# Optimization experiments

Measured on AMD Instinct MI355X. Metric: run time of the kernel, lower is better.

Reference implementation:

```python
import jax, jax.numpy as jnp
import numpy as np

B, N, H, DH = 2, 512, 12, 64
DIM, DPAIR, DCOND = 768, 128, 512
INNER = 4 * DIM  # expansion_factor * dim


def _ln(x, eps=1e-5):
    m = jnp.mean(x, -1, keepdims=True)
    v = jnp.mean((x - m) ** 2, -1, keepdims=True)
    return (x - m) * jax.lax.rsqrt(v + eps)


def _rope(t):
    # t: [b,h,n,d]; standard rotary over head dim
    d = t.shape[-1]
    pos = jnp.arange(t.shape[2], dtype=t.dtype)
    inv = 1.0 / (10000.0 ** (jnp.arange(0, d, 2, dtype=t.dtype) / d))
    ang = pos[:, None] * inv[None, :]  # [n, d/2]
    cos, sin = jnp.cos(ang), jnp.sin(ang)
    t1, t2 = t[..., 0::2], t[..., 1::2]
    return jnp.stack([t1 * cos - t2 * sin, t1 * sin + t2 * cos], -1).reshape(t.shape)


def _adaln(x, cond, mask, gw, gb, bw):
    cn = _ln(cond)
    return (_ln(x) * jax.nn.sigmoid(cn @ gw + gb) + cn @ bw) * mask[..., None]


def _scale_out(x, cond, mask, w, b):
    # adaLN-zero style output scaling
    return x * jax.nn.sigmoid(_ln(cond) @ w + b) * mask[..., None]


def _windowed_attn(q, k, v, bias, pair_mask, n_queries, n_keys):
    # q/k/v: [b,h,n,d]; bias: [b,h,n,n]; pair_mask: [b,n,n]
    b, h, n, d = q.shape
    nw = n // n_queries
    centers = jnp.arange(nw) * n_queries + n_queries // 2
    idx = centers[:, None] - n_keys // 2 + jnp.arange(n_keys)[None, :]  # [nw,nk]
    valid = (idx >= 0) & (idx < n)
    idxc = jnp.clip(idx, 0, n - 1)
    qw = q.reshape(b, h, nw, n_queries, d)
    kw = k[:, :, idxc]  # [b,h,nw,nk,d]
    vw = v[:, :, idxc]
    ib = jnp.broadcast_to(idxc[None, None, :, None, :], (b, h, nw, n_queries, n_keys))
    bias_w = jnp.take_along_axis(bias.reshape(b, h, nw, n_queries, n), ib, axis=-1)
    pm = jnp.take_along_axis(
        pair_mask.reshape(b, nw, n_queries, n),
        jnp.broadcast_to(idxc[None, :, None, :], (b, nw, n_queries, n_keys)), axis=-1)
    scores = jnp.einsum('bhwqd,bhwkd->bhwqk', qw, kw) / jnp.sqrt(jnp.asarray(d, q.dtype)) + bias_w
    ok = (pm[:, None] > 0) & valid[None, None, :, None, :]
    attn = jax.nn.softmax(jnp.where(ok, scores, -1e9), axis=-1)
    out = jnp.einsum('bhwqk,bhwkd->bhwqd', attn, vw)
    return out.reshape(b, h, n, d)


def setup_inputs() -> dict:
    key = jax.random.key(0)
    ks = iter(jax.random.split(key, 48))
    nrm = lambda shape: jax.random.normal(next(ks), shape, jnp.float32) * 0.02
    return dict(
        x=jax.random.normal(next(ks), (B, N, DIM), jnp.float32),
        pair_rep=jax.random.normal(next(ks), (B, N, N, DPAIR), jnp.float32),
        cond=jax.random.normal(next(ks), (B, N, DCOND), jnp.float32),
        mask=jnp.ones((B, N), jnp.float32),
        pair_mask=jnp.ones((B, N, N), jnp.float32),
        adaln1_gw=nrm((DCOND, DIM)), adaln1_gb=jnp.zeros((DIM,), jnp.float32), adaln1_bw=nrm((DCOND, DIM)),
        wq=nrm((DIM, H * DH)), bq=jnp.zeros((H * DH,), jnp.float32),
        wk=nrm((DIM, H * DH)), bk=jnp.zeros((H * DH,), jnp.float32),
        wv=nrm((DIM, H * DH)), bv=jnp.zeros((H * DH,), jnp.float32),
        wg=nrm((DIM, H * DH)), bg=jnp.zeros((H * DH,), jnp.float32),
        wb_pair=nrm((DPAIR, H)),
        wo=nrm((H * DH, DIM)), bo=jnp.zeros((DIM,), jnp.float32),
        scale1_w=nrm((DCOND, DIM)), scale1_b=jnp.full((DIM,), -2.0, jnp.float32),
        adaln2_gw=nrm((DCOND, DIM)), adaln2_gb=jnp.zeros((DIM,), jnp.float32), adaln2_bw=nrm((DCOND, DIM)),
        tr_win=nrm((DIM, 2 * INNER)), tr_wout=nrm((INNER, DIM)),
        scale2_w=nrm((DCOND, DIM)), scale2_b=jnp.full((DIM,), -2.0, jnp.float32),
        n_queries=32, n_keys=128,
    )


def reference(x, pair_rep, cond, mask, pair_mask,
              adaln1_gw, adaln1_gb, adaln1_bw,
              wq, bq, wk, bk, wv, bv, wg, bg, wb_pair, wo, bo,
              scale1_w, scale1_b,
              adaln2_gw, adaln2_gb, adaln2_bw,
              tr_win, tr_wout,
              scale2_w, scale2_b,
              n_queries, n_keys):
    b, n, _ = x.shape
    x = x * mask[..., None]

    # --- MHA (adaLN -> pair-biased rotary windowed attention -> adaLN-zero scale) ---
    xa = _adaln(x, cond, mask, adaln1_gw, adaln1_gb, adaln1_bw)
    q = (xa @ wq + bq).reshape(b, n, H, DH).transpose(0, 2, 1, 3)
    k = (xa @ wk + bk).reshape(b, n, H, DH).transpose(0, 2, 1, 3)
    v = (xa @ wv + bv).reshape(b, n, H, DH).transpose(0, 2, 1, 3)
    q, k = _ln(q), _ln(k)      # qk layernorm
    q, k = _rope(q), _rope(k)  # rotary
    bias = jnp.einsum('bijp,ph->bhij', _ln(pair_rep), wb_pair)
    o = _windowed_attn(q, k, v, bias, pair_mask, n_queries, n_keys)
    o = o.transpose(0, 2, 1, 3).reshape(b, n, H * DH)
    attn_out = (o * jax.nn.sigmoid(xa @ wg + bg)) @ wo + bo
    attn_out = _scale_out(attn_out, cond, mask, scale1_w, scale1_b) * mask[..., None]
    x = (attn_out + x) * mask[..., None]  # residual_mha

    # --- Transition (adaLN -> SwiGLU -> adaLN-zero scale) ---
    xt = _adaln(x, cond, mask, adaln2_gw, adaln2_gb, adaln2_bw)
    a, g = jnp.split(xt @ tr_win, 2, axis=-1)
    tr = ((a * jax.nn.silu(g)) @ tr_wout) * mask[..., None]
    tr = _scale_out(tr, cond, mask, scale2_w, scale2_b) * mask[..., None]
    x = (tr + x) * mask[..., None]  # residual_transition
    return x * mask[..., None]
```

## Files before the change

kernel.cpp:

```cpp
#include <hip/hip_runtime.h>
#include <hip/hip_bf16.h>
#include <math.h>
#include <stdint.h>

#define Bc   2
#define Nc   512
#define Hc   12
#define DHc  64
#define DIMc 768
#define DPAIRc 128
#define DCONDc 512
#define INNERc 3072
#define NQc  32
#define NKc  128
#define NWc  (Nc / NQc)

typedef __attribute__((ext_vector_type(8))) short short8;
typedef __attribute__((ext_vector_type(4))) float floatx4;

__device__ inline float wave_sum(float v) {
#pragma unroll
  for (int off = 32; off > 0; off >>= 1) v += __shfl_xor(v, off, 64);
  return v;
}
__device__ inline float wave_max(float v) {
#pragma unroll
  for (int off = 32; off > 0; off >>= 1) v = fmaxf(v, __shfl_xor(v, off, 64));
  return v;
}
__device__ inline float block_sum(float v, float* red) {
  v = wave_sum(v);
  int wv = threadIdx.x >> 6, lane = threadIdx.x & 63;
  __syncthreads();
  if (lane == 0) red[wv] = v;
  __syncthreads();
  return red[0] + red[1] + red[2] + red[3];
}
__device__ inline float sigmoidf(float x) { return 1.0f / (1.0f + expf(-x)); }

__device__ __forceinline__ void gload16(const void* g, void* l) {
  __builtin_amdgcn_global_load_lds(
      reinterpret_cast<__attribute__((address_space(1))) const void*>(
          reinterpret_cast<uintptr_t>(g)),
      reinterpret_cast<__attribute__((address_space(3))) void*>(
          static_cast<uint32_t>(reinterpret_cast<uintptr_t>(l))),
      16, 0, 0);
}

__global__ __launch_bounds__(256) void ln_rows_bf16_k(const float* __restrict__ in,
                                                      __hip_bfloat16* __restrict__ out, int C) {
  __shared__ float red[4];
  int row = blockIdx.x;
  const float* x = in + (size_t)row * C;
  float s = 0.f;
  for (int c = threadIdx.x; c < C; c += 256) s += x[c];
  float mean = block_sum(s, red) / C;
  float vs = 0.f;
  for (int c = threadIdx.x; c < C; c += 256) { float d = x[c] - mean; vs += d * d; }
  float var = block_sum(vs, red) / C;
  float r = rsqrtf(var + 1e-5f);
  for (int c = threadIdx.x; c < C; c += 256)
    out[(size_t)row * C + c] = __float2bfloat16((x[c] - mean) * r);
}

struct TP6 { const float* s0; const float* s1; const float* s2;
             const float* s3; const float* s4; const float* s5; };
__global__ __launch_bounds__(256) void transpose_cast_batch_k(TP6 p,
    __hip_bfloat16* __restrict__ dstBase, int K, int N, int interleave) {
  __shared__ float tile[32][33];
  const float* srcs[6] = {p.s0, p.s1, p.s2, p.s3, p.s4, p.s5};
  const float* src = srcs[blockIdx.z];
  __hip_bfloat16* dst = dstBase + (size_t)blockIdx.z * K * N;
  int k0 = blockIdx.y * 32, n0 = blockIdx.x * 32;
  int t = threadIdx.x;
  int r = t >> 5, c = t & 31;
#pragma unroll
  for (int i = 0; i < 4; ++i) tile[r + i * 8][c] = src[(size_t)(k0 + r + i * 8) * N + n0 + c];
  __syncthreads();
#pragma unroll
  for (int i = 0; i < 4; ++i) {
    int n = n0 + r + i * 8;
    int dr = n;
    if (interleave) {
      int half = N >> 1;
      dr = (n < half) ? (((n >> 4) << 5) + (n & 15))
                      : ((((n - half) >> 4) << 5) + 16 + ((n - half) & 15));
    }
    dst[(size_t)dr * K + k0 + c] = __float2bfloat16(tile[c][r + i * 8]);
  }
}

__global__ __launch_bounds__(256) void concat_bias_k(
    const float* __restrict__ a1_gb, const float* __restrict__ s1_b,
    const float* __restrict__ a2_gb, const float* __restrict__ s2_b,
    const float* __restrict__ bq, const float* __restrict__ bk,
    const float* __restrict__ bv, const float* __restrict__ bg,
    const float* __restrict__ wb_pair,
    float* __restrict__ cb6, float* __restrict__ bqkvg,
    __hip_bfloat16* __restrict__ wbT, float* __restrict__ colsum) {
  int i = blockIdx.x * 256 + threadIdx.x;
  if (i < 6 * DIMc) {
    int seg = i / DIMc, o = i - seg * DIMc;
    float v = 0.f;
    if (seg == 0) v = a1_gb[o];
    else if (seg == 2) v = s1_b[o];
    else if (seg == 3) v = a2_gb[o];
    else if (seg == 5) v = s2_b[o];
    cb6[i] = v;
  }
  if (i < 4 * DIMc) {
    int seg = i / DIMc, o = i - seg * DIMc;
    bqkvg[i] = (seg == 0) ? bq[o] : (seg == 1) ? bk[o] : (seg == 2) ? bv[o] : bg[o];
  }
  if (i < 16 * DPAIRc) {
    int h = i >> 7, c = i & 127;
    wbT[i] = (h < Hc) ? __float2bfloat16(wb_pair[c * Hc + h]) : __float2bfloat16(0.f);
  }
  if (blockIdx.x == 0 && threadIdx.x < 16) {
    int h = threadIdx.x;
    float s = 0.f;
    if (h < Hc)
      for (int c = 0; c < DPAIRc; ++c)
        s += __bfloat162float(__float2bfloat16(wb_pair[c * Hc + h]));
    colsum[h] = s;
  }
}

template <int WNT>
__global__ __launch_bounds__(256) void gemm_bf16_k(
    const __hip_bfloat16* __restrict__ A, const __hip_bfloat16* __restrict__ Bt,
    float* __restrict__ C, int M, int N, int K,
    const float* __restrict__ bias,
    const float* __restrict__ ss, int ssst,
    const float* __restrict__ resid, const float* __restrict__ maskp, int mode) {
  constexpr int TN = 32 * WNT;
  __shared__ __align__(16) __hip_bfloat16 As[2][128 * 32];
  __shared__ __align__(16) __hip_bfloat16 Bs[2][TN * 32];
  int tid = threadIdx.x;
  int lane = tid & 63, wv = tid >> 6;
  int l16 = lane & 15, quad = lane >> 4;
  int m0 = blockIdx.y * 128, n0 = blockIdx.x * TN;
  int wm0 = (wv >> 1) * 64, wn0 = (wv & 1) * (16 * WNT);

  int srow = tid >> 2;
  int skc = (tid & 3) * 8;
  const __hip_bfloat16* Ab  = A  + (size_t)(m0 + srow) * K + skc;
  const __hip_bfloat16* Ab2 = Ab + (size_t)64 * K;
  const __hip_bfloat16* Bb  = Bt + (size_t)(n0 + srow) * K + skc;
  const __hip_bfloat16* Bb2 = Bb + (size_t)64 * K;
  __hip_bfloat16* AsW0 = &As[0][0] + wv * 512;
  __hip_bfloat16* AsW1 = &As[1][0] + wv * 512;
  __hip_bfloat16* BsW0 = &Bs[0][0] + wv * 512;
  __hip_bfloat16* BsW1 = &Bs[1][0] + wv * 512;

  floatx4 acc[4][WNT];
#pragma unroll
  for (int mi = 0; mi < 4; ++mi)
#pragma unroll
    for (int nj = 0; nj < WNT; ++nj) acc[mi][nj] = (floatx4){0.f, 0.f, 0.f, 0.f};

  auto stage = [&](int kk, __hip_bfloat16* AW, __hip_bfloat16* BW) {
    gload16(Ab + kk, AW);
    gload16(Ab2 + kk, AW + 2048);
    if (WNT == 4) {
      gload16(Bb + kk, BW);
      gload16(Bb2 + kk, BW + 2048);
    } else {
      if (wv < 2) gload16(Bb + kk, BW);
    }
  };
  auto compute = [&](const __hip_bfloat16* Asb, const __hip_bfloat16* Bsb) {
    short8 a[4], b[WNT];
#pragma unroll
    for (int mi = 0; mi < 4; ++mi)
      a[mi] = *(const short8*)(const void*)&Asb[(wm0 + mi * 16 + l16) * 32 + quad * 8];
#pragma unroll
    for (int nj = 0; nj < WNT; ++nj)
      b[nj] = *(const short8*)(const void*)&Bsb[(wn0 + nj * 16 + l16) * 32 + quad * 8];
#pragma unroll
    for (int mi = 0; mi < 4; ++mi)
#pragma unroll
      for (int nj = 0; nj < WNT; ++nj)
        acc[mi][nj] = __builtin_amdgcn_mfma_f32_16x16x32_bf16(a[mi], b[nj], acc[mi][nj], 0, 0, 0);
  };

  stage(0, AsW0, BsW0);
  __syncthreads();
  for (int k0 = 0; k0 < K; k0 += 64) {
    if (k0 + 32 < K) stage(k0 + 32, AsW1, BsW1);
    compute(&As[0][0], &Bs[0][0]);
    __syncthreads();
    if (k0 + 64 < K) stage(k0 + 64, AsW0, BsW0);
    compute(&As[1][0], &Bs[1][0]);
    __syncthreads();
  }

  if (mode == 3) {
    if constexpr (WNT >= 2) {
      __hip_bfloat16* Cb = (__hip_bfloat16*)C;
      int halfN = N >> 1;
#pragma unroll
      for (int mi = 0; mi < 4; ++mi) {
#pragma unroll
        for (int njp = 0; njp < WNT / 2; ++njp) {
          int outcol = ((n0 + wn0) >> 1) + njp * 16 + l16;
#pragma unroll
          for (int r = 0; r < 4; ++r) {
            int m = m0 + wm0 + mi * 16 + quad * 4 + r;
            float av = acc[mi][2 * njp][r];
            float gv = acc[mi][2 * njp + 1][r];
            Cb[(size_t)m * halfN + outcol] = __float2bfloat16(av * gv * sigmoidf(gv));
          }
        }
      }
    }
    return;
  }

#pragma unroll
  for (int mi = 0; mi < 4; ++mi) {
#pragma unroll
    for (int nj = 0; nj < WNT; ++nj) {
      int ncol = n0 + wn0 + nj * 16 + l16;
      float bb = bias ? bias[ncol] : 0.f;
#pragma unroll
      for (int r = 0; r < 4; ++r) {
        int m = m0 + wm0 + mi * 16 + quad * 4 + r;
        float v = acc[mi][nj][r] + bb;
        if (mode == 1) {
          float mk = maskp[m];
          v *= sigmoidf(ss[(size_t)m * ssst + ncol]) * mk * mk;
          v = (v + resid[(size_t)m * N + ncol]) * mk;
        } else if (mode == 2) {
          float mk = maskp[m];
          v = v * mk * sigmoidf(ss[(size_t)m * ssst + ncol]) * mk * mk;
          v = (v + resid[(size_t)m * N + ncol]) * mk * mk;
        }
        C[(size_t)m * N + ncol] = v;
      }
    }
  }
}

__global__ __launch_bounds__(256) void adaln_apply_k(
    const float* __restrict__ xin, const float* __restrict__ maskp,
    const float* __restrict__ graw, const float* __restrict__ braw, int ssst,
    __hip_bfloat16* __restrict__ xa, float* __restrict__ xm) {
  __shared__ float red[4];
  int row = blockIdx.x;
  float mk = maskp[row];
  const float* xr = xin + (size_t)row * DIMc;
  float vals[3];
  float s = 0.f;
#pragma unroll
  for (int it = 0; it < 3; ++it) {
    int c = threadIdx.x + it * 256;
    float v = xr[c] * mk;
    vals[it] = v;
    s += v;
  }
  float mean = block_sum(s, red) * (1.0f / DIMc);
  float vs = 0.f;
#pragma unroll
  for (int it = 0; it < 3; ++it) { float d = vals[it] - mean; vs += d * d; }
  float var = block_sum(vs, red) * (1.0f / DIMc);
  float r = rsqrtf(var + 1e-5f);
#pragma unroll
  for (int it = 0; it < 3; ++it) {
    int c = threadIdx.x + it * 256;
    size_t sidx = (size_t)row * ssst + c;
    if (xm) xm[(size_t)row * DIMc + c] = vals[it];
    float o = ((vals[it] - mean) * r * sigmoidf(graw[sidx]) + braw[sidx]) * mk;
    xa[(size_t)row * DIMc + c] = __float2bfloat16(o);
  }
}

__global__ __launch_bounds__(256) void pair_bias_mfma_k(
    const float* __restrict__ pr, const __hip_bfloat16* __restrict__ wbT,
    const float* __restrict__ colsum, float* __restrict__ biasw) {
  constexpr int LDR = 136;
  __shared__ __hip_bfloat16 rows[128 * LDR];
  __shared__ float meanS[128];
  __shared__ float rstdS[128];
  int bi = blockIdx.x;
  int i = bi & (Nc - 1), b = bi >> 9;
  int w = i >> 5, qi = i & 31;
  int j0 = w * NQc - 48;
  int t = threadIdx.x;
  int sub = t >> 5;
  int c4 = t & 31;
  const float* prb = pr + (size_t)bi * (Nc * DPAIRc);
#pragma unroll
  for (int step = 0; step < 16; ++step) {
    int row = step * 8 + sub;
    int jc = min(max(j0 + row, 0), Nc - 1);
    float4 v = *(const float4*)(prb + (size_t)jc * DPAIRc + c4 * 4);
    union { __hip_bfloat16 h[4]; uint2 u; } pk;
    pk.h[0] = __float2bfloat16(v.x); pk.h[1] = __float2bfloat16(v.y);
    pk.h[2] = __float2bfloat16(v.z); pk.h[3] = __float2bfloat16(v.w);
    *(uint2*)(void*)&rows[row * LDR + c4 * 4] = pk.u;
    float s = v.x + v.y + v.z + v.w;
    float s2 = v.x * v.x + v.y * v.y + v.z * v.z + v.w * v.w;
#pragma unroll
    for (int off = 16; off > 0; off >>= 1) {
      s += __shfl_xor(s, off, 64);
      s2 += __shfl_xor(s2, off, 64);
    }
    if (c4 == 0) {
      float mean = s * (1.0f / 128.0f);
      float var = s2 * (1.0f / 128.0f) - mean * mean;
      meanS[row] = mean;
      rstdS[row] = rsqrtf(var + 1e-5f);
    }
  }
  __syncthreads();
  int lane = t & 63, wv = t >> 6;
  int l16 = lane & 15, quad = lane >> 4;
  short8 bfrag[4];
#pragma unroll
  for (int ks = 0; ks < 4; ++ks)
    bfrag[ks] = *(const short8*)(const void*)&wbT[l16 * 128 + ks * 32 + quad * 8];
  float cs = colsum[l16];
#pragma unroll
  for (int mt = 0; mt < 2; ++mt) {
    int mtile = wv * 2 + mt;
    floatx4 acc = (floatx4){0.f, 0.f, 0.f, 0.f};
#pragma unroll
    for (int ks = 0; ks < 4; ++ks) {
      short8 a = *(const short8*)(const void*)&rows[(mtile * 16 + l16) * LDR + ks * 32 + quad * 8];
      acc = __builtin_amdgcn_mfma_f32_16x16x32_bf16(a, bfrag[ks], acc, 0, 0, 0);
    }
    if (l16 < Hc) {
      int m0r = mtile * 16 + quad * 4;
      float4 ov;
      float* po = &ov.x;
#pragma unroll
      for (int r = 0; r < 4; ++r) {
        int m = m0r + r;
        po[r] = rstdS[m] * (acc[r] - meanS[m] * cs);
      }
      *(float4*)&biasw[((((size_t)(b * Hc + l16)) * NWc + w) * NQc + qi) * NKc + m0r] = ov;
    }
  }
}

__global__ __launch_bounds__(256) void wattn_k(
    const float* __restrict__ qkvg, const float* __restrict__ biasw,
    const float* __restrict__ pair_mask, __hip_bfloat16* __restrict__ o) {
  constexpr int LQ = 72;
  constexpr int LV = 136;
  constexpr int LS = 132;
  constexpr int LP = 136;
  __shared__ __hip_bfloat16 qs[32 * LQ];
  __shared__ __hip_bfloat16 ks[128 * LQ];
  __shared__ __hip_bfloat16 vT[64 * LV];
  __shared__ float sc[32 * LS];
  __shared__ __hip_bfloat16 scP[32 * LP];
  const int QS = 4 * DIMc;
  int blk = blockIdx.x;
  int w = blk & (NWc - 1);
  int bh = blk >> 4;
  int h = bh % Hc;
  int b = bh / Hc;
  int t = threadIdx.x;
  int j0 = w * NQc - 48;
  for (int e = t; e < 512; e += 256) {
    int qrow = e >> 4, c4 = e & 15;
    float4 v = *(const float4*)&qkvg[(size_t)(b * Nc + w * NQc + qrow) * QS + h * DHc + c4 * 4];
    float s = v.x + v.y + v.z + v.w;
    float s2 = v.x * v.x + v.y * v.y + v.z * v.z + v.w * v.w;
#pragma unroll
    for (int off = 1; off < 16; off <<= 1) {
      s += __shfl_xor(s, off, 64);
      s2 += __shfl_xor(s2, off, 64);
    }
    float mean = s * (1.0f / 64.0f);
    float rr = rsqrtf(s2 * (1.0f / 64.0f) - mean * mean + 1e-5f);
    float qn0 = (v.x - mean) * rr, qn1 = (v.y - mean) * rr;
    float qn2 = (v.z - mean) * rr, qn3 = (v.w - mean) * rr;
    float pos = (float)(w * NQc + qrow);
    float inv0 = exp2f(-(float)(c4 * 2) * 0.415241011861f);
    float inv1 = exp2f(-(float)(c4 * 2 + 1) * 0.415241011861f);
    float a0 = pos * inv0, a1 = pos * inv1;
    float c0 = cosf(a0), sn0 = sinf(a0), c1 = cosf(a1), sn1 = sinf(a1);
    union { __hip_bfloat16 hh[4]; uint2 u; } pk;
    pk.hh[0] = __float2bfloat16(qn0 * c0 - qn1 * sn0);
    pk.hh[1] = __float2bfloat16(qn0 * sn0 + qn1 * c0);
    pk.hh[2] = __float2bfloat16(qn2 * c1 - qn3 * sn1);
    pk.hh[3] = __float2bfloat16(qn2 * sn1 + qn3 * c1);
    *(uint2*)(void*)&qs[qrow * LQ + c4 * 4] = pk.u;
  }
  for (int e = t; e < 2048; e += 256) {
    int kk = e >> 4, c4 = e & 15;
    int jc = min(max(j0 + kk, 0), Nc - 1);
    size_t src = (size_t)(b * Nc + jc) * QS + h * DHc + c4 * 4;
    float4 kv = *(const float4*)&qkvg[src + DIMc];
    float4 vv = *(const float4*)&qkvg[src + 2 * DIMc];
    float s = kv.x + kv.y + kv.z + kv.w;
    float s2 = kv.x * kv.x + kv.y * kv.y + kv.z * kv.z + kv.w * kv.w;
#pragma unroll
    for (int off = 1; off < 16; off <<= 1) {
      s += __shfl_xor(s, off, 64);
      s2 += __shfl_xor(s2, off, 64);
    }
    float mean = s * (1.0f / 64.0f);
    float rr = rsqrtf(s2 * (1.0f / 64.0f) - mean * mean + 1e-5f);
    float kn0 = (kv.x - mean) * rr, kn1 = (kv.y - mean) * rr;
    float kn2 = (kv.z - mean) * rr, kn3 = (kv.w - mean) * rr;
    float pos = (float)jc;
    float inv0 = exp2f(-(float)(c4 * 2) * 0.415241011861f);
    float inv1 = exp2f(-(float)(c4 * 2 + 1) * 0.415241011861f);
    float a0 = pos * inv0, a1 = pos * inv1;
    float c0 = cosf(a0), sn0 = sinf(a0), c1 = cosf(a1), sn1 = sinf(a1);
    union { __hip_bfloat16 hh[4]; uint2 u; } pk;
    pk.hh[0] = __float2bfloat16(kn0 * c0 - kn1 * sn0);
    pk.hh[1] = __float2bfloat16(kn0 * sn0 + kn1 * c0);
    pk.hh[2] = __float2bfloat16(kn2 * c1 - kn3 * sn1);
    pk.hh[3] = __float2bfloat16(kn2 * sn1 + kn3 * c1);
    *(uint2*)(void*)&ks[kk * LQ + c4 * 4] = pk.u;
    vT[(c4 * 4 + 0) * LV + kk] = __float2bfloat16(vv.x);
    vT[(c4 * 4 + 1) * LV + kk] = __float2bfloat16(vv.y);
    vT[(c4 * 4 + 2) * LV + kk] = __float2bfloat16(vv.z);
    vT[(c4 * 4 + 3) * LV + kk] = __float2bfloat16(vv.w);
  }
  for (int e = t; e < 4096; e += 256) {
    int qrow = e >> 7, key = e & 127;
    int j = j0 + key;
    bool valid = (j >= 0) && (j < Nc);
    int jc = min(max(j, 0), Nc - 1);
    float pm = pair_mask[((size_t)(b * Nc + w * NQc + qrow)) * Nc + jc];
    bool ok = valid && (pm > 0.f);
    sc[qrow * LS + key] = ok ? biasw[((size_t)blk * 32 + qrow) * 128 + key] : -1e30f;
  }
  __syncthreads();
  int lane = t & 63, wv = t >> 6;
  int l16 = lane & 15, quad = lane >> 4;
  {
    short8 bfr[2][2];
#pragma unroll
    for (int nt = 0; nt < 2; ++nt)
#pragma unroll
      for (int k2 = 0; k2 < 2; ++k2)
        bfr[nt][k2] = *(const short8*)(const void*)&ks[(wv * 32 + nt * 16 + l16) * LQ + k2 * 32 + quad * 8];
#pragma unroll
    for (int mi = 0; mi < 2; ++mi) {
      short8 afr[2];
#pragma unroll
      for (int k2 = 0; k2 < 2; ++k2)
        afr[k2] = *(const short8*)(const void*)&qs[(mi * 16 + l16) * LQ + k2 * 32 + quad * 8];
#pragma unroll
      for (int nt = 0; nt < 2; ++nt) {
        floatx4 acc = (floatx4){0.f, 0.f, 0.f, 0.f};
        acc = __builtin_amdgcn_mfma_f32_16x16x32_bf16(afr[0], bfr[nt][0], acc, 0, 0, 0);
        acc = __builtin_amdgcn_mfma_f32_16x16x32_bf16(afr[1], bfr[nt][1], acc, 0, 0, 0);
        int key = wv * 32 + nt * 16 + l16;
#pragma unroll
        for (int r = 0; r < 4; ++r) {
          int m = mi * 16 + quad * 4 + r;
          float sv = sc[m * LS + key];
          if (sv > -1e29f) sc[m * LS + key] = sv + acc[r] * 0.125f;
        }
      }
    }
  }
  __syncthreads();
#pragma unroll
  for (int rr = 0; rr < 8; ++rr) {
    int qq = wv * 8 + rr;
    float v0 = sc[qq * LS + lane], v1 = sc[qq * LS + 64 + lane];
    float mx = wave_max(fmaxf(v0, v1));
    float e0 = expf(v0 - mx), e1 = expf(v1 - mx);
    float inv = 1.0f / wave_sum(e0 + e1);
    scP[qq * LP + lane] = __float2bfloat16(e0 * inv);
    scP[qq * LP + 64 + lane] = __float2bfloat16(e1 * inv);
  }
  __syncthreads();
  {
    short8 vb[4];
#pragma unroll
    for (int k4 = 0; k4 < 4; ++k4)
      vb[k4] = *(const short8*)(const void*)&vT[(wv * 16 + l16) * LV + k4 * 32 + quad * 8];
#pragma unroll
    for (int mi = 0; mi < 2; ++mi) {
      floatx4 acc = (floatx4){0.f, 0.f, 0.f, 0.f};
#pragma unroll
      for (int k4 = 0; k4 < 4; ++k4) {
        short8 pa = *(const short8*)(const void*)&scP[(mi * 16 + l16) * LP + k4 * 32 + quad * 8];
        acc = __builtin_amdgcn_mfma_f32_16x16x32_bf16(pa, vb[k4], acc, 0, 0, 0);
      }
      int d = wv * 16 + l16;
#pragma unroll
      for (int r = 0; r < 4; ++r) {
        int m = mi * 16 + quad * 4 + r;
        size_t mrow = (size_t)(b * Nc + w * NQc + m);
        float g = qkvg[mrow * QS + 3 * DIMc + h * DHc + d];
        o[mrow * DIMc + h * DHc + d] = __float2bfloat16(acc[r] * sigmoidf(g));
      }
    }
  }
}

extern "C" void kernel_launch(void* const* d_in, const int* in_sizes, int n_in,
                              void* d_out, int out_size, void* d_ws, size_t ws_size,
                              hipStream_t stream) {
  const float* x        = (const float*)d_in[0];
  const float* pair_rep = (const float*)d_in[1];
  const float* cond     = (const float*)d_in[2];
  const float* mask     = (const float*)d_in[3];
  const float* pair_mask= (const float*)d_in[4];
  const float* a1_gw    = (const float*)d_in[5];
  const float* a1_gb    = (const float*)d_in[6];
  const float* a1_bw    = (const float*)d_in[7];
  const float* wq       = (const float*)d_in[8];
  const float* bq       = (const float*)d_in[9];
  const float* wk       = (const float*)d_in[10];
  const float* bk       = (const float*)d_in[11];
  const float* wv       = (const float*)d_in[12];
  const float* bv       = (const float*)d_in[13];
  const float* wg       = (const float*)d_in[14];
  const float* bg       = (const float*)d_in[15];
  const float* wb_pair  = (const float*)d_in[16];
  const float* wo       = (const float*)d_in[17];
  const float* bo       = (const float*)d_in[18];
  const float* s1_w     = (const float*)d_in[19];
  const float* s1_b     = (const float*)d_in[20];
  const float* a2_gw    = (const float*)d_in[21];
  const float* a2_gb    = (const float*)d_in[22];
  const float* a2_bw    = (const float*)d_in[23];
  const float* tr_win   = (const float*)d_in[24];
  const float* tr_wout  = (const float*)d_in[25];
  const float* s2_w     = (const float*)d_in[26];
  const float* s2_b     = (const float*)d_in[27];
  float* out = (float*)d_out;

  const int M = Bc * Nc;
  char* wsb = (char*)d_ws;
  size_t off = 0;
  auto alloc = [&](size_t bytes) { void* p = wsb + off; off += (bytes + 255) & ~(size_t)255; return p; };

  __hip_bfloat16* cnb     = (__hip_bfloat16*)alloc((size_t)M * DCONDc * 2);
  __hip_bfloat16* Wc6t    = (__hip_bfloat16*)alloc((size_t)6 * DIMc * DCONDc * 2);
  __hip_bfloat16* Wqkvg5t = (__hip_bfloat16*)alloc((size_t)5 * DIMc * DIMc * 2);
  __hip_bfloat16* twint   = (__hip_bfloat16*)alloc((size_t)2 * INNERc * DIMc * 2);
  __hip_bfloat16* twoutt  = (__hip_bfloat16*)alloc((size_t)DIMc * INNERc * 2);
  float* cb6    = (float*)alloc((size_t)6 * DIMc * 4);
  float* bqkvg  = (float*)alloc((size_t)4 * DIMc * 4);
  __hip_bfloat16* wbT = (__hip_bfloat16*)alloc((size_t)16 * DPAIRc * 2);
  float* colsum = (float*)alloc(16 * 4);
  float* proj_c = (float*)alloc((size_t)M * 6 * DIMc * 4);
  float* xm     = (float*)alloc((size_t)M * DIMc * 4);
  __hip_bfloat16* xa = (__hip_bfloat16*)alloc((size_t)M * DIMc * 2);
  float* qkvg   = (float*)alloc((size_t)M * 4 * DIMc * 4);
  float* biasw  = (float*)alloc((size_t)Bc * Hc * NWc * NQc * NKc * 4);
  __hip_bfloat16* obg = (__hip_bfloat16*)alloc((size_t)M * DIMc * 2);
  float* x2     = (float*)alloc((size_t)M * DIMc * 4);
  __hip_bfloat16* xt = (__hip_bfloat16*)alloc((size_t)M * DIMc * 2);
  __hip_bfloat16* actb = (__hip_bfloat16*)alloc((size_t)M * INNERc * 2);
  __hip_bfloat16* wot = Wqkvg5t + (size_t)4 * DIMc * DIMc;
  (void)ws_size; (void)in_sizes; (void)n_in; (void)out_size;

  dim3 blk(256);

  ln_rows_bf16_k<<<M, blk, 0, stream>>>(cond, cnb, DCONDc);

  transpose_cast_batch_k<<<dim3(DIMc / 32, DCONDc / 32, 6), blk, 0, stream>>>(
      TP6{a1_gw, a1_bw, s1_w, a2_gw, a2_bw, s2_w}, Wc6t, DCONDc, DIMc, 0);
  transpose_cast_batch_k<<<dim3(DIMc / 32, DIMc / 32, 5), blk, 0, stream>>>(
      TP6{wq, wk, wv, wg, wo, wo}, Wqkvg5t, DIMc, DIMc, 0);
  transpose_cast_batch_k<<<dim3(2 * INNERc / 32, DIMc / 32, 1), blk, 0, stream>>>(
      TP6{tr_win, tr_win, tr_win, tr_win, tr_win, tr_win}, twint, DIMc, 2 * INNERc, 1);
  transpose_cast_batch_k<<<dim3(DIMc / 32, INNERc / 32, 1), blk, 0, stream>>>(
      TP6{tr_wout, tr_wout, tr_wout, tr_wout, tr_wout, tr_wout}, twoutt, INNERc, DIMc, 0);

  concat_bias_k<<<(6 * DIMc + 255) / 256, blk, 0, stream>>>(
      a1_gb, s1_b, a2_gb, s2_b, bq, bk, bv, bg, wb_pair, cb6, bqkvg, wbT, colsum);

  gemm_bf16_k<4><<<dim3(6 * DIMc / 128, M / 128), blk, 0, stream>>>(
      cnb, Wc6t, proj_c, M, 6 * DIMc, DCONDc, cb6, nullptr, 0, nullptr, nullptr, 0);

  adaln_apply_k<<<M, blk, 0, stream>>>(x, mask, proj_c + 0, proj_c + DIMc, 6 * DIMc, xa, xm);

  gemm_bf16_k<4><<<dim3(4 * DIMc / 128, M / 128), blk, 0, stream>>>(
      xa, Wqkvg5t, qkvg, M, 4 * DIMc, DIMc, bqkvg, nullptr, 0, nullptr, nullptr, 0);

  pair_bias_mfma_k<<<Bc * Nc, blk, 0, stream>>>(pair_rep, wbT, colsum, biasw);

  wattn_k<<<Bc * Hc * NWc, blk, 0, stream>>>(qkvg, biasw, pair_mask, obg);

  gemm_bf16_k<1><<<dim3(DIMc / 32, M / 128), blk, 0, stream>>>(
      obg, wot, x2, M, DIMc, DIMc, bo, proj_c + 2 * DIMc, 6 * DIMc, xm, mask, 1);

  adaln_apply_k<<<M, blk, 0, stream>>>(x2, mask, proj_c + 3 * DIMc, proj_c + 4 * DIMc,
                                       6 * DIMc, xt, nullptr);

  gemm_bf16_k<4><<<dim3(2 * INNERc / 128, M / 128), blk, 0, stream>>>(
      xt, twint, (float*)actb, M, 2 * INNERc, DIMc, nullptr, nullptr, 0, nullptr, nullptr, 3);

  gemm_bf16_k<1><<<dim3(DIMc / 32, M / 128), blk, 0, stream>>>(
      actb, twoutt, out, M, DIMc, INNERc, nullptr, proj_c + 5 * DIMc, 6 * DIMc, x2, mask, 2);
}
```

Before: 590.0 us.

## Restructure GEMM k-loop to keep two stages in flight with explicit vmcnt waits

Replaces the double-buffered k-loop, which synchronized with __syncthreads after each stage, with a prefetch-two-ahead pipeline. Per-wave s_waitcnt vmcnt counts wait only for the current tile's direct-to-LDS loads, and sched_barriers pin the compute block between explicit s_barriers. The aim is to hide global-load latency behind MFMA work and avoid draining all outstanding loads at each barrier. The hard-coded vmcnt values depend on how many loads each wave issues per stage, so a miscount would cause races.

New measurement: 599.0 us. No clear change (+1.5%).

```diff
diff --git a/kernel.cpp b/kernel.cpp
--- a/kernel.cpp
+++ b/kernel.cpp
@@ -184,15 +184,31 @@
         acc[mi][nj] = __builtin_amdgcn_mfma_f32_16x16x32_bf16(a[mi], b[nj], acc[mi][nj], 0, 0, 0);
   };
 
+  int nt = K >> 5;
   stage(0, AsW0, BsW0);
-  __syncthreads();
-  for (int k0 = 0; k0 < K; k0 += 64) {
-    if (k0 + 32 < K) stage(k0 + 32, AsW1, BsW1);
-    compute(&As[0][0], &Bs[0][0]);
-    __syncthreads();
-    if (k0 + 64 < K) stage(k0 + 64, AsW0, BsW0);
-    compute(&As[1][0], &Bs[1][0]);
-    __syncthreads();
+  stage(32, AsW1, BsW1);
+  for (int t = 0; t < nt; ++t) {
+    if (t < nt - 1) {
+      if (WNT == 4) {
+        asm volatile("s_waitcnt vmcnt(4)" ::: "memory");
+      } else {
+        if (wv < 2) asm volatile("s_waitcnt vmcnt(3)" ::: "memory");
+        else        asm volatile("s_waitcnt vmcnt(2)" ::: "memory");
+      }
+    } else {
+      asm volatile("s_waitcnt vmcnt(0)" ::: "memory");
+    }
+    __builtin_amdgcn_s_barrier();
+    __builtin_amdgcn_sched_barrier(0);
+    if (t & 1) compute(&As[1][0], &Bs[1][0]);
+    else       compute(&As[0][0], &Bs[0][0]);
+    __builtin_amdgcn_sched_barrier(0);
+    __builtin_amdgcn_s_barrier();
+    if (t + 2 < nt) {
+      int kk = (t + 2) << 5;
+      if (t & 1) stage(kk, AsW1, BsW1);
+      else       stage(kk, AsW0, BsW0);
+    }
   }
 
   if (mode == 3) {
```

## Merge preprocessing kernels into one launch and precompute a RoPE table

Applied to the files above, without the earlier changes.

Folds the separate cond layernorm, four weight transpose/cast launches and the bias-concat kernel into a single prep kernel whose blocks branch on index ranges. The same kernel also fills a cos/sin RoPE table, which the windowed attention kernel now reads instead of calling exp2f/cosf/sinf per element for q and k. This cuts kernel launch count and removes repeated transcendental work in attention. The cost is an extra small global buffer and table reads, plus one heterogeneous kernel whose branches may diverge in shape and load balance.

New measurement: 568.2 us. -3.7%, faster.

```diff
diff --git a/kernel.cpp b/kernel.cpp
--- a/kernel.cpp
+++ b/kernel.cpp
@@ -47,32 +47,28 @@
       16, 0, 0);
 }
 
-__global__ __launch_bounds__(256) void ln_rows_bf16_k(const float* __restrict__ in,
-                                                      __hip_bfloat16* __restrict__ out, int C) {
-  __shared__ float red[4];
-  int row = blockIdx.x;
-  const float* x = in + (size_t)row * C;
-  float s = 0.f;
-  for (int c = threadIdx.x; c < C; c += 256) s += x[c];
-  float mean = block_sum(s, red) / C;
-  float vs = 0.f;
-  for (int c = threadIdx.x; c < C; c += 256) { float d = x[c] - mean; vs += d * d; }
-  float var = block_sum(vs, red) / C;
-  float r = rsqrtf(var + 1e-5f);
-  for (int c = threadIdx.x; c < C; c += 256)
-    out[(size_t)row * C + c] = __float2bfloat16((x[c] - mean) * r);
-}
-
-struct TP6 { const float* s0; const float* s1; const float* s2;
-             const float* s3; const float* s4; const float* s5; };
-__global__ __launch_bounds__(256) void transpose_cast_batch_k(TP6 p,
-    __hip_bfloat16* __restrict__ dstBase, int K, int N, int interleave) {
-  __shared__ float tile[32][33];
-  const float* srcs[6] = {p.s0, p.s1, p.s2, p.s3, p.s4, p.s5};
-  const float* src = srcs[blockIdx.z];
-  __hip_bfloat16* dst = dstBase + (size_t)blockIdx.z * K * N;
-  int k0 = blockIdx.y * 32, n0 = blockIdx.x * 32;
-  int t = threadIdx.x;
+struct PrepArgs {
+  const float *a1_gw, *a1_bw, *s1_w, *a2_gw, *a2_bw, *s2_w;
+  const float *wq, *wk, *wv, *wg, *wo;
+  const float *tr_win, *tr_wout;
+  const float *cond;
+  const float *a1_gb, *s1_b, *a2_gb, *s2_b;
+  const float *bq, *bk, *bv, *bg, *wb_pair;
+  __hip_bfloat16 *Wc6t, *Wqkvg5t, *twint, *twoutt, *cnb, *wbT;
+  float *cb6, *bqkvg, *colsum, *rope;
+};
+
+#define PR_T1 2304
+#define PR_T2 (PR_T1 + 2880)
+#define PR_T3 (PR_T2 + 4608)
+#define PR_T4 (PR_T3 + 2304)
+#define PR_LN (PR_T4 + 1024)
+#define PR_CB (PR_LN + 18)
+#define PR_RT (PR_CB + 64)
+
+__device__ __forceinline__ void do_transpose(float (*tile)[33], const float* __restrict__ src,
+    __hip_bfloat16* __restrict__ dst, int K, int N, int bxx, int byy, int interleave, int t) {
+  int k0 = byy * 32, n0 = bxx * 32;
   int r = t >> 5, c = t & 31;
 #pragma unroll
   for (int i = 0; i < 4; ++i) tile[r + i * 8][c] = src[(size_t)(k0 + r + i * 8) * N + n0 + c];
@@ -90,39 +86,73 @@
   }
 }
 
-__global__ __launch_bounds__(256) void concat_bias_k(
-    const float* __restrict__ a1_gb, const float* __restrict__ s1_b,
-    const float* __restrict__ a2_gb, const float* __restrict__ s2_b,
-    const float* __restrict__ bq, const float* __restrict__ bk,
-    const float* __restrict__ bv, const float* __restrict__ bg,
-    const float* __restrict__ wb_pair,
-    float* __restrict__ cb6, float* __restrict__ bqkvg,
-    __hip_bfloat16* __restrict__ wbT, float* __restrict__ colsum) {
-  int i = blockIdx.x * 256 + threadIdx.x;
-  if (i < 6 * DIMc) {
-    int seg = i / DIMc, o = i - seg * DIMc;
-    float v = 0.f;
-    if (seg == 0) v = a1_gb[o];
-    else if (seg == 2) v = s1_b[o];
-    else if (seg == 3) v = a2_gb[o];
-    else if (seg == 5) v = s2_b[o];
-    cb6[i] = v;
-  }
-  if (i < 4 * DIMc) {
-    int seg = i / DIMc, o = i - seg * DIMc;
-    bqkvg[i] = (seg == 0) ? bq[o] : (seg == 1) ? bk[o] : (seg == 2) ? bv[o] : bg[o];
-  }
-  if (i < 16 * DPAIRc) {
-    int h = i >> 7, c = i & 127;
-    wbT[i] = (h < Hc) ? __float2bfloat16(wb_pair[c * Hc + h]) : __float2bfloat16(0.f);
-  }
-  if (blockIdx.x == 0 && threadIdx.x < 16) {
-    int h = threadIdx.x;
-    float s = 0.f;
-    if (h < Hc)
-      for (int c = 0; c < DPAIRc; ++c)
-        s += __bfloat162float(__float2bfloat16(wb_pair[c * Hc + h]));
-    colsum[h] = s;
+__global__ __launch_bounds__(256) void prep_k(PrepArgs p) {
+  __shared__ float tile[32][33];
+  __shared__ float red[4];
+  int bx = blockIdx.x, t = threadIdx.x;
+  if (bx < PR_T1) {
+    int z = bx / 384, rem = bx - z * 384;
+    int by = rem / 24, bxx = rem - by * 24;
+    const float* srcs[6] = {p.a1_gw, p.a1_bw, p.s1_w, p.a2_gw, p.a2_bw, p.s2_w};
+    do_transpose(tile, srcs[z], p.Wc6t + (size_t)z * DIMc * DCONDc, DCONDc, DIMc, bxx, by, 0, t);
+  } else if (bx < PR_T2) {
+    int l = bx - PR_T1;
+    int z = l / 576, rem = l - z * 576;
+    int by = rem / 24, bxx = rem - by * 24;
+    const float* srcs[5] = {p.wq, p.wk, p.wv, p.wg, p.wo};
+    do_transpose(tile, srcs[z], p.Wqkvg5t + (size_t)z * DIMc * DIMc, DIMc, DIMc, bxx, by, 0, t);
+  } else if (bx < PR_T3) {
+    int l = bx - PR_T2;
+    int by = l / 192, bxx = l - by * 192;
+    do_transpose(tile, p.tr_win, p.twint, DIMc, 2 * INNERc, bxx, by, 1, t);
+  } else if (bx < PR_T4) {
+    int l = bx - PR_T3;
+    int by = l / 24, bxx = l - by * 24;
+    do_transpose(tile, p.tr_wout, p.twoutt, INNERc, DIMc, bxx, by, 0, t);
+  } else if (bx < PR_LN) {
+    int row = bx - PR_T4;
+    const float* x = p.cond + (size_t)row * DCONDc;
+    float v0 = x[t], v1 = x[t + 256];
+    float mean = block_sum(v0 + v1, red) * (1.0f / DCONDc);
+    float d0 = v0 - mean, d1 = v1 - mean;
+    float var = block_sum(d0 * d0 + d1 * d1, red) * (1.0f / DCONDc);
+    float r = rsqrtf(var + 1e-5f);
+    p.cnb[(size_t)row * DCONDc + t] = __float2bfloat16(d0 * r);
+    p.cnb[(size_t)row * DCONDc + t + 256] = __float2bfloat16(d1 * r);
+  } else if (bx < PR_CB) {
+    int lb = bx - PR_LN;
+    int i = lb * 256 + t;
+    if (i < 6 * DIMc) {
+      int seg = i / DIMc, o = i - seg * DIMc;
+      float v = 0.f;
+      if (seg == 0) v = p.a1_gb[o];
+      else if (seg == 2) v = p.s1_b[o];
+      else if (seg == 3) v = p.a2_gb[o];
+      else if (seg == 5) v = p.s2_b[o];
+      p.cb6[i] = v;
+    }
+    if (i < 4 * DIMc) {
+      int seg = i / DIMc, o = i - seg * DIMc;
+      p.bqkvg[i] = (seg == 0) ? p.bq[o] : (seg == 1) ? p.bk[o] : (seg == 2) ? p.bv[o] : p.bg[o];
+    }
+    if (i < 16 * DPAIRc) {
+      int h = i >> 7, c = i & 127;
+      p.wbT[i] = (h < Hc) ? __float2bfloat16(p.wb_pair[c * Hc + h]) : __float2bfloat16(0.f);
+    }
+    if (lb == 0 && t < 16) {
+      int h = t;
+      float s = 0.f;
+      if (h < Hc)
+        for (int c = 0; c < DPAIRc; ++c)
+          s += __bfloat162float(__float2bfloat16(p.wb_pair[c * Hc + h]));
+      p.colsum[h] = s;
+    }
+  } else {
+    int idx = (bx - PR_CB) * 256 + t;
+    int pos = idx >> 5, i = idx & 31;
+    float ang = (float)pos * exp2f(-(float)i * 0.415241011861f);
+    p.rope[idx * 2] = cosf(ang);
+    p.rope[idx * 2 + 1] = sinf(ang);
   }
 }
 
@@ -346,7 +376,8 @@
 
 __global__ __launch_bounds__(256) void wattn_k(
     const float* __restrict__ qkvg, const float* __restrict__ biasw,
-    const float* __restrict__ pair_mask, __hip_bfloat16* __restrict__ o) {
+    const float* __restrict__ pair_mask, const float* __restrict__ rope,
+    __hip_bfloat16* __restrict__ o) {
   constexpr int LQ = 72;
   constexpr int LV = 136;
   constexpr int LS = 132;
@@ -378,16 +409,12 @@
     float rr = rsqrtf(s2 * (1.0f / 64.0f) - mean * mean + 1e-5f);
     float qn0 = (v.x - mean) * rr, qn1 = (v.y - mean) * rr;
     float qn2 = (v.z - mean) * rr, qn3 = (v.w - mean) * rr;
-    float pos = (float)(w * NQc + qrow);
-    float inv0 = exp2f(-(float)(c4 * 2) * 0.415241011861f);
-    float inv1 = exp2f(-(float)(c4 * 2 + 1) * 0.415241011861f);
-    float a0 = pos * inv0, a1 = pos * inv1;
-    float c0 = cosf(a0), sn0 = sinf(a0), c1 = cosf(a1), sn1 = sinf(a1);
+    float4 cs4 = *(const float4*)&rope[(size_t)(w * NQc + qrow) * 64 + c4 * 4];
     union { __hip_bfloat16 hh[4]; uint2 u; } pk;
-    pk.hh[0] = __float2bfloat16(qn0 * c0 - qn1 * sn0);
-    pk.hh[1] = __float2bfloat16(qn0 * sn0 + qn1 * c0);
-    pk.hh[2] = __float2bfloat16(qn2 * c1 - qn3 * sn1);
-    pk.hh[3] = __float2bfloat16(qn2 * sn1 + qn3 * c1);
+    pk.hh[0] = __float2bfloat16(qn0 * cs4.x - qn1 * cs4.y);
+    pk.hh[1] = __float2bfloat16(qn0 * cs4.y + qn1 * cs4.x);
+    pk.hh[2] = __float2bfloat16(qn2 * cs4.z - qn3 * cs4.w);
+    pk.hh[3] = __float2bfloat16(qn2 * cs4.w + qn3 * cs4.z);
     *(uint2*)(void*)&qs[qrow * LQ + c4 * 4] = pk.u;
   }
   for (int e = t; e < 2048; e += 256) {
@@ -407,16 +434,12 @@
     float rr = rsqrtf(s2 * (1.0f / 64.0f) - mean * mean + 1e-5f);
     float kn0 = (kv.x - mean) * rr, kn1 = (kv.y - mean) * rr;
     float kn2 = (kv.z - mean) * rr, kn3 = (kv.w - mean) * rr;
-    float pos = (float)jc;
-    float inv0 = exp2f(-(float)(c4 * 2) * 0.415241011861f);
-    float inv1 = exp2f(-(float)(c4 * 2 + 1) * 0.415241011861f);
-    float a0 = pos * inv0, a1 = pos * inv1;
-    float c0 = cosf(a0), sn0 = sinf(a0), c1 = cosf(a1), sn1 = sinf(a1);
+    float4 cs4 = *(const float4*)&rope[(size_t)jc * 64 + c4 * 4];
     union { __hip_bfloat16 hh[4]; uint2 u; } pk;
-    pk.hh[0] = __float2bfloat16(kn0 * c0 - kn1 * sn0);
-    pk.hh[1] = __float2bfloat16(kn0 * sn0 + kn1 * c0);
-    pk.hh[2] = __float2bfloat16(kn2 * c1 - kn3 * sn1);
-    pk.hh[3] = __float2bfloat16(kn2 * sn1 + kn3 * c1);
+    pk.hh[0] = __float2bfloat16(kn0 * cs4.x - kn1 * cs4.y);
+    pk.hh[1] = __float2bfloat16(kn0 * cs4.y + kn1 * cs4.x);
+    pk.hh[2] = __float2bfloat16(kn2 * cs4.z - kn3 * cs4.w);
+    pk.hh[3] = __float2bfloat16(kn2 * cs4.w + kn3 * cs4.z);
     *(uint2*)(void*)&ks[kk * LQ + c4 * 4] = pk.u;
     vT[(c4 * 4 + 0) * LV + kk] = __float2bfloat16(vv.x);
     vT[(c4 * 4 + 1) * LV + kk] = __float2bfloat16(vv.y);
@@ -547,6 +570,7 @@
   float* bqkvg  = (float*)alloc((size_t)4 * DIMc * 4);
   __hip_bfloat16* wbT = (__hip_bfloat16*)alloc((size_t)16 * DPAIRc * 2);
   float* colsum = (float*)alloc(16 * 4);
+  float* rope   = (float*)alloc((size_t)Nc * 64 * 4);
   float* proj_c = (float*)alloc((size_t)M * 6 * DIMc * 4);
   float* xm     = (float*)alloc((size_t)M * DIMc * 4);
   __hip_bfloat16* xa = (__hip_bfloat16*)alloc((size_t)M * DIMc * 2);
@@ -561,19 +585,18 @@
 
   dim3 blk(256);
 
-  ln_rows_bf16_k<<<M, blk, 0, stream>>>(cond, cnb, DCONDc);
-
-  transpose_cast_batch_k<<<dim3(DIMc / 32, DCONDc / 32, 6), blk, 0, stream>>>(
-      TP6{a1_gw, a1_bw, s1_w, a2_gw, a2_bw, s2_w}, Wc6t, DCONDc, DIMc, 0);
-  transpose_cast_batch_k<<<dim3(DIMc / 32, DIMc / 32, 5), blk, 0, stream>>>(
-      TP6{wq, wk, wv, wg, wo, wo}, Wqkvg5t, DIMc, DIMc, 0);
-  transpose_cast_batch_k<<<dim3(2 * INNERc / 32, DIMc / 32, 1), blk, 0, stream>>>(
-      TP6{tr_win, tr_win, tr_win, tr_win, tr_win, tr_win}, twint, DIMc, 2 * INNERc, 1);
-  transpose_cast_batch_k<<<dim3(DIMc / 32, INNERc / 32, 1), blk, 0, stream>>>(
-      TP6{tr_wout, tr_wout, tr_wout, tr_wout, tr_wout, tr_wout}, twoutt, INNERc, DIMc, 0);
-
-  concat_bias_k<<<(6 * DIMc + 255) / 256, blk, 0, stream>>>(
-      a1_gb, s1_b, a2_gb, s2_b, bq, bk, bv, bg, wb_pair, cb6, bqkvg, wbT, colsum);
+  PrepArgs pa;
+  pa.a1_gw = a1_gw; pa.a1_bw = a1_bw; pa.s1_w = s1_w;
+  pa.a2_gw = a2_gw; pa.a2_bw = a2_bw; pa.s2_w = s2_w;
+  pa.wq = wq; pa.wk = wk; pa.wv = wv; pa.wg = wg; pa.wo = wo;
+  pa.tr_win = tr_win; pa.tr_wout = tr_wout;
+  pa.cond = cond;
+  pa.a1_gb = a1_gb; pa.s1_b = s1_b; pa.a2_gb = a2_gb; pa.s2_b = s2_b;
+  pa.bq = bq; pa.bk = bk; pa.bv = bv; pa.bg = bg; pa.wb_pair = wb_pair;
+  pa.Wc6t = Wc6t; pa.Wqkvg5t = Wqkvg5t; pa.twint = twint; pa.twoutt = twoutt;
+  pa.cnb = cnb; pa.wbT = wbT;
+  pa.cb6 = cb6; pa.bqkvg = bqkvg; pa.colsum = colsum; pa.rope = rope;
+  prep_k<<<PR_RT, blk, 0, stream>>>(pa);
 
   gemm_bf16_k<4><<<dim3(6 * DIMc / 128, M / 128), blk, 0, stream>>>(
       cnb, Wc6t, proj_c, M, 6 * DIMc, DCONDc, cb6, nullptr, 0, nullptr, nullptr, 0);
@@ -585,7 +608,7 @@
 
   pair_bias_mfma_k<<<Bc * Nc, blk, 0, stream>>>(pair_rep, wbT, colsum, biasw);
 
-  wattn_k<<<Bc * Hc * NWc, blk, 0, stream>>>(qkvg, biasw, pair_mask, obg);
+  wattn_k<<<Bc * Hc * NWc, blk, 0, stream>>>(qkvg, biasw, pair_mask, rope, obg);
 
   gemm_bf16_k<1><<<dim3(DIMc / 32, M / 128), blk, 0, stream>>>(
       obg, wot, x2, M, DIMc, DIMc, bo, proj_c + 2 * DIMc, 6 * DIMc, xm, mask, 1);
```
